# Performance work log

Hardware: AMD Instinct MI355X
Metric: run time of the kernel (lower is better)

Reference implementation:

```python
import jax, jax.numpy as jnp
import numpy as np

ED = 1024
NH = 16
HD = ED // NH


def setup_inputs() -> dict:
    key = jax.random.key(0)
    ks = jax.random.split(key, 9)
    s = 1.0 / np.sqrt(ED)
    return {
        "x": jax.random.normal(ks[0], (2, 2048, ED), dtype=jnp.float32),
        "wq": jax.random.uniform(ks[1], (ED, ED), jnp.float32, -s, s),
        "bq": jax.random.uniform(ks[2], (ED,), jnp.float32, -s, s),
        "wk": jax.random.uniform(ks[3], (ED, ED), jnp.float32, -s, s),
        "bk": jax.random.uniform(ks[4], (ED,), jnp.float32, -s, s),
        "wv": jax.random.uniform(ks[5], (ED, ED), jnp.float32, -s, s),
        "bv": jax.random.uniform(ks[6], (ED,), jnp.float32, -s, s),
        "wo": jax.random.uniform(ks[7], (ED, ED), jnp.float32, -s, s),
        "bo": jax.random.uniform(ks[8], (ED,), jnp.float32, -s, s),
    }


def reference(x, wq, bq, wk, bk, wv, bv, wo, bo):
    B, N, _ = x.shape
    # projections; weights stored as [out, in] like nn.Linear -> x @ W.T + b
    def proj(w, b):
        y = jnp.einsum('bnd,ed->bne', x, w) + b
        return y.reshape(B, N, NH, HD).transpose(0, 2, 1, 3)  # [B, H, N, hd]
    Q, K, V = proj(wq, bq), proj(wk, bk), proj(wv, bv)
    scores = jnp.einsum('bhnd,bhmd->bhnm', Q, K) / jnp.sqrt(jnp.float32(HD))
    attn = jax.nn.softmax(scores, axis=-1)
    ctx = jnp.einsum('bhnm,bhmd->bhnd', attn, V)
    ctx = ctx.transpose(0, 2, 1, 3).reshape(B, N, ED)
    return jnp.einsum('bne,de->bnd', ctx, wo) + bo
```

## Files before the change

### kernel.cpp

```cpp
#include <hip/hip_runtime.h>
#include <hip/hip_bf16.h>

#define ED 1024
#define NH 16
#define HD 64
#define SEQ 2048

typedef float f32x4 __attribute__((ext_vector_type(4)));
typedef float f32x16 __attribute__((ext_vector_type(16)));
typedef short s16x8 __attribute__((ext_vector_type(8)));
typedef short s16x4 __attribute__((ext_vector_type(4)));
typedef __attribute__((address_space(1))) const unsigned int GBuf;
typedef __attribute__((address_space(3))) unsigned int LBuf;

#define QSC 0.18033688011112042f

union BF8 { s16x8 v; __hip_bfloat16 h[8]; };

__device__ __forceinline__ unsigned cvt_pk_bf16(float lo, float hi) {
  unsigned r;
  asm("v_cvt_pk_bf16_f32 %0, %1, %2" : "=v"(r) : "v"(lo), "v"(hi));
  return r;
}

__device__ __forceinline__ s16x8 pack_pfrag(float p0, float p1, float p2, float p3,
                                            float p4, float p5, float p6, float p7) {
  unsigned w0 = cvt_pk_bf16(p0, p1), w1 = cvt_pk_bf16(p2, p3);
  unsigned w2 = cvt_pk_bf16(p4, p5), w3 = cvt_pk_bf16(p6, p7);
  asm("v_permlane32_swap_b32 %0, %1" : "+v"(w0), "+v"(w2));
  asm("v_permlane32_swap_b32 %0, %1" : "+v"(w1), "+v"(w3));
  union { unsigned u[4]; s16x8 v; } r;
  r.u[0] = w0; r.u[1] = w1; r.u[2] = w2; r.u[3] = w3;
  return r.v;
}

__device__ inline void cvt_one(const float* __restrict__ s, __hip_bfloat16* __restrict__ d,
                               int n, int t, int stride) {
  const int n8 = n >> 3;
  for (int i = t; i < n8; i += stride) {
    const float4 u = ((const float4*)s)[2 * i];
    const float4 v = ((const float4*)s)[2 * i + 1];
    BF8 o;
    o.h[0] = __float2bfloat16(u.x); o.h[1] = __float2bfloat16(u.y);
    o.h[2] = __float2bfloat16(u.z); o.h[3] = __float2bfloat16(u.w);
    o.h[4] = __float2bfloat16(v.x); o.h[5] = __float2bfloat16(v.y);
    o.h[6] = __float2bfloat16(v.z); o.h[7] = __float2bfloat16(v.w);
    ((s16x8*)d)[i] = o.v;
  }
}

__global__ __launch_bounds__(256) void cvt5(const float* s0, const float* s1, const float* s2,
                                            const float* s3, const float* s4,
                                            __hip_bfloat16* d0, __hip_bfloat16* d1,
                                            __hip_bfloat16* d2, __hip_bfloat16* d3,
                                            __hip_bfloat16* d4,
                                            int n0, int n1, int n2, int n3, int n4) {
  const int stride = gridDim.x * blockDim.x;
  const int t = blockIdx.x * blockDim.x + threadIdx.x;
  cvt_one(s0, d0, n0, t, stride);
  cvt_one(s1, d1, n1, t, stride);
  cvt_one(s2, d2, n2, t, stride);
  cvt_one(s3, d3, n3, t, stride);
  cvt_one(s4, d4, n4, t, stride);
}

__global__ __launch_bounds__(256) void gemm_qkv(const __hip_bfloat16* __restrict__ A,
                                                const __hip_bfloat16* __restrict__ wq,
                                                const float* __restrict__ bq,
                                                const __hip_bfloat16* __restrict__ wk,
                                                const float* __restrict__ bk,
                                                const __hip_bfloat16* __restrict__ wv,
                                                const float* __restrict__ bv,
                                                __hip_bfloat16* __restrict__ Qo,
                                                __hip_bfloat16* __restrict__ Ko,
                                                __hip_bfloat16* __restrict__ Vo) {
  __shared__ __hip_bfloat16 As[128 * 64];
  __shared__ __hip_bfloat16 Bs[128 * 64];

  const int z = blockIdx.z;
  const __hip_bfloat16* W = (z == 0) ? wq : (z == 1) ? wk : wv;
  const float* bias = (z == 0) ? bq : (z == 1) ? bk : bv;

  const int tid = threadIdx.x;
  const int wave = tid >> 6, lane = tid & 63;
  const int ln15 = lane & 15, lg = lane >> 4;
  const int m0 = blockIdx.y * 128, n0 = blockIdx.x * 128;
  const int wr = (wave >> 1) * 64, wc = (wave & 1) * 64;

  f32x4 acc[4][4];
#pragma unroll
  for (int i = 0; i < 4; i++)
#pragma unroll
    for (int j = 0; j < 4; j++) acc[i][j] = (f32x4){0.f, 0.f, 0.f, 0.f};

  const int srow = tid >> 3;
  const int sk = (tid & 7) * 8;

  for (int k0 = 0; k0 < ED; k0 += 64) {
    __syncthreads();
#pragma unroll
    for (int c = 0; c < 4; c++) {
      const int r = c * 32 + srow;
      __builtin_amdgcn_global_load_lds((GBuf*)(A + (size_t)(m0 + r) * ED + k0 + sk),
                                       (LBuf*)((char*)As + c * 4096 + tid * 16), 16, 0, 0);
    }
#pragma unroll
    for (int c = 0; c < 4; c++) {
      const int r = c * 32 + srow;
      __builtin_amdgcn_global_load_lds((GBuf*)(W + (size_t)(n0 + r) * ED + k0 + sk),
                                       (LBuf*)((char*)Bs + c * 4096 + tid * 16), 16, 0, 0);
    }
    __syncthreads();
#pragma unroll
    for (int kb = 0; kb < 2; kb++) {
      const int kof = kb * 32 + lg * 8;
      s16x8 a[4], b[4];
#pragma unroll
      for (int i = 0; i < 4; i++)
        a[i] = *(const s16x8*)&As[(wr + i * 16 + ln15) * 64 + kof];
#pragma unroll
      for (int j = 0; j < 4; j++)
        b[j] = *(const s16x8*)&Bs[(wc + j * 16 + ln15) * 64 + kof];
#pragma unroll
      for (int i = 0; i < 4; i++)
#pragma unroll
        for (int j = 0; j < 4; j++)
          acc[i][j] = __builtin_amdgcn_mfma_f32_16x16x32_bf16(a[i], b[j], acc[i][j], 0, 0, 0);
    }
  }

  const float scale = (z == 0) ? QSC : 1.0f;
  if (z < 2) {
    __hip_bfloat16* out = (z == 0) ? Qo : Ko;
#pragma unroll
    for (int j = 0; j < 4; j++) {
      const int e = n0 + wc + j * 16 + ln15;
      const float bvv = bias[e];
      const int h = e >> 6, hd = e & 63;
#pragma unroll
      for (int i = 0; i < 4; i++) {
#pragma unroll
        for (int r = 0; r < 4; r++) {
          const int m = m0 + wr + i * 16 + lg * 4 + r;
          const int b = m >> 11, n = m & 2047;
          out[(((size_t)(b * NH + h)) * SEQ + n) * HD + hd] =
              __float2bfloat16((acc[i][j][r] + bvv) * scale);
        }
      }
    }
  } else {
#pragma unroll
    for (int j = 0; j < 4; j++) {
      const int e = n0 + wc + j * 16 + ln15;
      const float bvv = bias[e];
      const int h = e >> 6, hd = e & 63;
#pragma unroll
      for (int i = 0; i < 4; i++) {
        const int m = m0 + wr + i * 16 + lg * 4;
        const int b = m >> 11, n = m & 2047;
        union { s16x4 v; __hip_bfloat16 hh[4]; } pk;
#pragma unroll
        for (int r = 0; r < 4; r++) pk.hh[r] = __float2bfloat16(acc[i][j][r] + bvv);
        *(s16x4*)&Vo[(((size_t)(b * NH + h)) * HD + hd) * SEQ + n] = pk.v;
      }
    }
  }
}

__global__ __launch_bounds__(256) void gemm_out(const __hip_bfloat16* __restrict__ A,
                                                const __hip_bfloat16* __restrict__ W,
                                                const float* __restrict__ bias,
                                                float* __restrict__ out) {
  __shared__ __hip_bfloat16 As[128 * 64];
  __shared__ __hip_bfloat16 Bs[128 * 64];

  const int tid = threadIdx.x;
  const int wave = tid >> 6, lane = tid & 63;
  const int ln15 = lane & 15, lg = lane >> 4;
  const int m0 = blockIdx.y * 128, n0 = blockIdx.x * 128;
  const int wr = (wave >> 1) * 64, wc = (wave & 1) * 64;

  f32x4 acc[4][4];
#pragma unroll
  for (int i = 0; i < 4; i++)
#pragma unroll
    for (int j = 0; j < 4; j++) acc[i][j] = (f32x4){0.f, 0.f, 0.f, 0.f};

  const int srow = tid >> 3;
  const int sk = (tid & 7) * 8;

  for (int k0 = 0; k0 < ED; k0 += 64) {
    __syncthreads();
#pragma unroll
    for (int c = 0; c < 4; c++) {
      const int r = c * 32 + srow;
      __builtin_amdgcn_global_load_lds((GBuf*)(A + (size_t)(m0 + r) * ED + k0 + sk),
                                       (LBuf*)((char*)As + c * 4096 + tid * 16), 16, 0, 0);
    }
#pragma unroll
    for (int c = 0; c < 4; c++) {
      const int r = c * 32 + srow;
      __builtin_amdgcn_global_load_lds((GBuf*)(W + (size_t)(n0 + r) * ED + k0 + sk),
                                       (LBuf*)((char*)Bs + c * 4096 + tid * 16), 16, 0, 0);
    }
    __syncthreads();
#pragma unroll
    for (int kb = 0; kb < 2; kb++) {
      const int kof = kb * 32 + lg * 8;
      s16x8 a[4], b[4];
#pragma unroll
      for (int i = 0; i < 4; i++)
        a[i] = *(const s16x8*)&As[(wr + i * 16 + ln15) * 64 + kof];
#pragma unroll
      for (int j = 0; j < 4; j++)
        b[j] = *(const s16x8*)&Bs[(wc + j * 16 + ln15) * 64 + kof];
#pragma unroll
      for (int i = 0; i < 4; i++)
#pragma unroll
        for (int j = 0; j < 4; j++)
          acc[i][j] = __builtin_amdgcn_mfma_f32_16x16x32_bf16(a[i], b[j], acc[i][j], 0, 0, 0);
    }
  }

#pragma unroll
  for (int j = 0; j < 4; j++) {
    const int e = n0 + wc + j * 16 + ln15;
    const float bvv = bias[e];
#pragma unroll
    for (int i = 0; i < 4; i++)
#pragma unroll
      for (int r = 0; r < 4; r++) {
        const int m = m0 + wr + i * 16 + lg * 4 + r;
        out[(size_t)m * ED + e] = acc[i][j][r] + bvv;
      }
  }
}

__global__ __launch_bounds__(256) void attn_bf16(const __hip_bfloat16* __restrict__ Q,
                                                 const __hip_bfloat16* __restrict__ K,
                                                 const __hip_bfloat16* __restrict__ VT,
                                                 __hip_bfloat16* __restrict__ CTX) {
  __shared__ __hip_bfloat16 KsS[2][64 * 64];
  __shared__ __hip_bfloat16 VtS[2][64 * 64];

  const int tid = threadIdx.x;
  const int wave = tid >> 6, lane = tid & 63;
  const int l31 = lane & 31, hi = lane >> 5;
  const int rswz = l31 & 7;

  const int bid = blockIdx.x;
  const int work = (bid & 7) * 64 + (bid >> 3);
  const int qb = work & 15;
  const int bh = work >> 4;

  const __hip_bfloat16* Qh = Q + (size_t)bh * SEQ * HD;
  const __hip_bfloat16* Kh = K + (size_t)bh * SEQ * HD;
  const __hip_bfloat16* Vh = VT + (size_t)bh * HD * SEQ;

  const int q0 = qb * 128 + wave * 32;

  s16x8 aq[4];
#pragma unroll
  for (int kb = 0; kb < 4; kb++)
    aq[kb] = *(const s16x8*)&Qh[(size_t)(q0 + l31) * HD + kb * 16 + hi * 8];

  f32x16 acc0 = {}, acc1 = {};
  float m_ = -1e30f, l_ = 0.f;

  auto STAGE = [&](int kt_, int buf_) {
#pragma unroll
    for (int c = 0; c < 2; c++) {
      const int row = c * 32 + (tid >> 3);
      const int colb = ((tid & 7) * 16) ^ ((row & 7) << 4);
      __builtin_amdgcn_global_load_lds(
          (GBuf*)((const char*)Kh + ((size_t)(kt_ * 64 + row) * HD) * 2 + colb),
          (LBuf*)((char*)&KsS[buf_][0] + c * 4096 + tid * 16), 16, 0, 0);
      __builtin_amdgcn_global_load_lds(
          (GBuf*)((const char*)Vh + ((size_t)row * SEQ + kt_ * 64) * 2 + colb),
          (LBuf*)((char*)&VtS[buf_][0] + c * 4096 + tid * 16), 16, 0, 0);
    }
  };

  STAGE(0, 0);

  const int NT = SEQ / 64;
  for (int kt = 0; kt < NT; kt++) {
    const int cur = kt & 1;
    __syncthreads();
    if (kt + 1 < NT) STAGE(kt + 1, cur ^ 1);

    f32x16 s0 = {}, s1 = {};
#pragma unroll
    for (int kb = 0; kb < 4; kb++) {
      const int coff = ((kb * 2 + hi) ^ rswz) << 4;
      const s16x8 ak0 = *(const s16x8*)((const char*)&KsS[cur][0] + l31 * 128 + coff);
      const s16x8 ak1 = *(const s16x8*)((const char*)&KsS[cur][0] + (32 + l31) * 128 + coff);
      s0 = __builtin_amdgcn_mfma_f32_32x32x16_bf16(ak0, aq[kb], s0, 0, 0, 0);
      s1 = __builtin_amdgcn_mfma_f32_32x32x16_bf16(ak1, aq[kb], s1, 0, 0, 0);
    }

    float t8[8];
#pragma unroll
    for (int i = 0; i < 8; i++)
      t8[i] = fmaxf(fmaxf(s0[i], s0[i + 8]), fmaxf(s1[i], s1[i + 8]));
    float tm = fmaxf(fmaxf(fmaxf(t8[0], t8[1]), fmaxf(t8[2], t8[3])),
                     fmaxf(fmaxf(t8[4], t8[5]), fmaxf(t8[6], t8[7])));
    tm = fmaxf(tm, __shfl_xor(tm, 32));

    if (!__all(tm - m_ <= 8.0f)) {
      const float mnew = fmaxf(m_, tm);
      const float fs = exp2f(m_ - mnew);
      m_ = mnew;
      l_ *= fs;
#pragma unroll
      for (int r = 0; r < 16; r++) { acc0[r] *= fs; acc1[r] *= fs; }
    }

#pragma unroll
    for (int r = 0; r < 16; r++) {
      s0[r] = exp2f(s0[r] - m_);
      s1[r] = exp2f(s1[r] - m_);
    }
    float sa[8];
#pragma unroll
    for (int i = 0; i < 8; i++) sa[i] = (s0[i] + s0[i + 8]) + (s1[i] + s1[i + 8]);
    float sum = ((sa[0] + sa[1]) + (sa[2] + sa[3])) + ((sa[4] + sa[5]) + (sa[6] + sa[7]));
    sum += __shfl_xor(sum, 32);
    l_ += sum;

    s16x8 pa[4];
    pa[0] = pack_pfrag(s0[0], s0[1], s0[2], s0[3], s0[4], s0[5], s0[6], s0[7]);
    pa[1] = pack_pfrag(s0[8], s0[9], s0[10], s0[11], s0[12], s0[13], s0[14], s0[15]);
    pa[2] = pack_pfrag(s1[0], s1[1], s1[2], s1[3], s1[4], s1[5], s1[6], s1[7]);
    pa[3] = pack_pfrag(s1[8], s1[9], s1[10], s1[11], s1[12], s1[13], s1[14], s1[15]);

#pragma unroll
    for (int kp = 0; kp < 4; kp++) {
      const int coff = ((kp * 2 + hi) ^ rswz) << 4;
      const s16x8 av0 = *(const s16x8*)((const char*)&VtS[cur][0] + l31 * 128 + coff);
      const s16x8 av1 = *(const s16x8*)((const char*)&VtS[cur][0] + (32 + l31) * 128 + coff);
      acc0 = __builtin_amdgcn_mfma_f32_32x32x16_bf16(av0, pa[kp], acc0, 0, 0, 0);
      acc1 = __builtin_amdgcn_mfma_f32_32x32x16_bf16(av1, pa[kp], acc1, 0, 0, 0);
    }
  }

  const float inv = 1.0f / l_;
  const int b = bh / NH, h = bh % NH;
  const int n = q0 + l31;
  __hip_bfloat16* dst = &CTX[((size_t)(b * SEQ + n)) * ED + h * HD];
#pragma unroll
  for (int g = 0; g < 4; g++) {
    union { s16x4 v; __hip_bfloat16 hh[4]; } p0, p1;
#pragma unroll
    for (int r = 0; r < 4; r++) {
      p0.hh[r] = __float2bfloat16(acc0[4 * g + r] * inv);
      p1.hh[r] = __float2bfloat16(acc1[4 * g + r] * inv);
    }
    *(s16x4*)&dst[8 * g + 4 * hi] = p0.v;
    *(s16x4*)&dst[32 + 8 * g + 4 * hi] = p1.v;
  }
}

extern "C" void kernel_launch(void* const* d_in, const int* in_sizes, int n_in,
                              void* d_out, int out_size, void* d_ws, size_t ws_size,
                              hipStream_t stream) {
  const float* x = (const float*)d_in[0];
  const float* wq = (const float*)d_in[1];
  const float* bq = (const float*)d_in[2];
  const float* wk = (const float*)d_in[3];
  const float* bk = (const float*)d_in[4];
  const float* wv = (const float*)d_in[5];
  const float* bv = (const float*)d_in[6];
  const float* wo = (const float*)d_in[7];
  const float* bo = (const float*)d_in[8];
  float* out = (float*)d_out;

  const int BN = in_sizes[0] / ED;

  char* w = (char*)d_ws;
  __hip_bfloat16* xbf = (__hip_bfloat16*)(w);
  __hip_bfloat16* wqb = (__hip_bfloat16*)(w + (8 << 20));
  __hip_bfloat16* wkb = (__hip_bfloat16*)(w + (10 << 20));
  __hip_bfloat16* wvb = (__hip_bfloat16*)(w + (12 << 20));
  __hip_bfloat16* wob = (__hip_bfloat16*)(w + (14 << 20));
  __hip_bfloat16* Qb = (__hip_bfloat16*)(w + (16 << 20));
  __hip_bfloat16* Kb = (__hip_bfloat16*)(w + (24 << 20));
  __hip_bfloat16* VTb = (__hip_bfloat16*)(w + (32 << 20));
  __hip_bfloat16* CTXb = (__hip_bfloat16*)(w + (40 << 20));

  cvt5<<<1024, 256, 0, stream>>>(x, wq, wk, wv, wo, xbf, wqb, wkb, wvb, wob,
                                 BN * ED, ED * ED, ED * ED, ED * ED, ED * ED);

  const dim3 blk(256);
  gemm_qkv<<<dim3(ED / 128, BN / 128, 3), blk, 0, stream>>>(
      xbf, wqb, bq, wkb, bk, wvb, bv, Qb, Kb, VTb);

  attn_bf16<<<dim3(512), blk, 0, stream>>>(Qb, Kb, VTb, CTXb);

  gemm_out<<<dim3(ED / 128, BN / 128), blk, 0, stream>>>(CTXb, wob, bo, out);
}
```

Measured before the change: 243.8 us.

## Double-buffer GEMM tiles, triple-buffer attention K/V, remap blocks, add wave priorities

Both projection GEMMs now double-buffer their A and B tiles in LDS, so the next k-tile loads while MFMAs run on the current one, with one barrier per iteration. Block indices are remapped so consecutive blocks share weight columns, aiming for better L2 reuse. The attention kernel moves to a three-stage K/V ring that prefetches two tiles ahead, using an explicit vmcnt wait and a raw barrier, and MFMA sections are wrapped in s_setprio. This doubles GEMM LDS use and raises attention LDS use, which can lower occupancy, and the hand-written vmcnt count must match the number of outstanding loads per stage.

```diff
diff --git a/kernel.cpp b/kernel.cpp
--- a/kernel.cpp
+++ b/kernel.cpp
@@ -74,17 +74,21 @@
                                                 __hip_bfloat16* __restrict__ Qo,
                                                 __hip_bfloat16* __restrict__ Ko,
                                                 __hip_bfloat16* __restrict__ Vo) {
-  __shared__ __hip_bfloat16 As[128 * 64];
-  __shared__ __hip_bfloat16 Bs[128 * 64];
-
-  const int z = blockIdx.z;
+  __shared__ __hip_bfloat16 As[2][128 * 64];
+  __shared__ __hip_bfloat16 Bs[2][128 * 64];
+
+  const int lin = (blockIdx.z * 32 + blockIdx.y) * 8 + blockIdx.x;
+  const int work = (lin & 7) * 96 + (lin >> 3);
+  const int z = work >> 8;
+  const int rem = work & 255;
+  const int m0 = (rem >> 3) * 128, n0 = (rem & 7) * 128;
+
   const __hip_bfloat16* W = (z == 0) ? wq : (z == 1) ? wk : wv;
   const float* bias = (z == 0) ? bq : (z == 1) ? bk : bv;
 
   const int tid = threadIdx.x;
   const int wave = tid >> 6, lane = tid & 63;
   const int ln15 = lane & 15, lg = lane >> 4;
-  const int m0 = blockIdx.y * 128, n0 = blockIdx.x * 128;
   const int wr = (wave >> 1) * 64, wc = (wave & 1) * 64;
 
   f32x4 acc[4][4];
@@ -96,37 +100,43 @@
   const int srow = tid >> 3;
   const int sk = (tid & 7) * 8;
 
-  for (int k0 = 0; k0 < ED; k0 += 64) {
-    __syncthreads();
+  auto STAGE = [&](int t, int buf) {
+    const int k0 = t * 64;
 #pragma unroll
     for (int c = 0; c < 4; c++) {
       const int r = c * 32 + srow;
       __builtin_amdgcn_global_load_lds((GBuf*)(A + (size_t)(m0 + r) * ED + k0 + sk),
-                                       (LBuf*)((char*)As + c * 4096 + tid * 16), 16, 0, 0);
-    }
-#pragma unroll
-    for (int c = 0; c < 4; c++) {
-      const int r = c * 32 + srow;
+                                       (LBuf*)((char*)&As[buf][0] + c * 4096 + tid * 16), 16, 0, 0);
       __builtin_amdgcn_global_load_lds((GBuf*)(W + (size_t)(n0 + r) * ED + k0 + sk),
-                                       (LBuf*)((char*)Bs + c * 4096 + tid * 16), 16, 0, 0);
-    }
-    __syncthreads();
+                                       (LBuf*)((char*)&Bs[buf][0] + c * 4096 + tid * 16), 16, 0, 0);
+    }
+  };
+
+  const int NT = ED / 64;
+  STAGE(0, 0);
+  __syncthreads();
+  for (int t = 0; t < NT; t++) {
+    const int cur = t & 1;
+    if (t + 1 < NT) STAGE(t + 1, cur ^ 1);
+    __builtin_amdgcn_s_setprio(1);
 #pragma unroll
     for (int kb = 0; kb < 2; kb++) {
       const int kof = kb * 32 + lg * 8;
       s16x8 a[4], b[4];
 #pragma unroll
       for (int i = 0; i < 4; i++)
-        a[i] = *(const s16x8*)&As[(wr + i * 16 + ln15) * 64 + kof];
+        a[i] = *(const s16x8*)&As[cur][(wr + i * 16 + ln15) * 64 + kof];
 #pragma unroll
       for (int j = 0; j < 4; j++)
-        b[j] = *(const s16x8*)&Bs[(wc + j * 16 + ln15) * 64 + kof];
+        b[j] = *(const s16x8*)&Bs[cur][(wc + j * 16 + ln15) * 64 + kof];
 #pragma unroll
       for (int i = 0; i < 4; i++)
 #pragma unroll
         for (int j = 0; j < 4; j++)
           acc[i][j] = __builtin_amdgcn_mfma_f32_16x16x32_bf16(a[i], b[j], acc[i][j], 0, 0, 0);
     }
+    __builtin_amdgcn_s_setprio(0);
+    __syncthreads();
   }
 
   const float scale = (z == 0) ? QSC : 1.0f;
@@ -171,13 +181,16 @@
                                                 const __hip_bfloat16* __restrict__ W,
                                                 const float* __restrict__ bias,
                                                 float* __restrict__ out) {
-  __shared__ __hip_bfloat16 As[128 * 64];
-  __shared__ __hip_bfloat16 Bs[128 * 64];
+  __shared__ __hip_bfloat16 As[2][128 * 64];
+  __shared__ __hip_bfloat16 Bs[2][128 * 64];
+
+  const int lin = blockIdx.y * 8 + blockIdx.x;
+  const int work = (lin & 7) * 32 + (lin >> 3);
+  const int m0 = (work >> 3) * 128, n0 = (work & 7) * 128;
 
   const int tid = threadIdx.x;
   const int wave = tid >> 6, lane = tid & 63;
   const int ln15 = lane & 15, lg = lane >> 4;
-  const int m0 = blockIdx.y * 128, n0 = blockIdx.x * 128;
   const int wr = (wave >> 1) * 64, wc = (wave & 1) * 64;
 
   f32x4 acc[4][4];
@@ -189,37 +202,43 @@
   const int srow = tid >> 3;
   const int sk = (tid & 7) * 8;
 
-  for (int k0 = 0; k0 < ED; k0 += 64) {
-    __syncthreads();
+  auto STAGE = [&](int t, int buf) {
+    const int k0 = t * 64;
 #pragma unroll
     for (int c = 0; c < 4; c++) {
       const int r = c * 32 + srow;
       __builtin_amdgcn_global_load_lds((GBuf*)(A + (size_t)(m0 + r) * ED + k0 + sk),
-                                       (LBuf*)((char*)As + c * 4096 + tid * 16), 16, 0, 0);
-    }
-#pragma unroll
-    for (int c = 0; c < 4; c++) {
-      const int r = c * 32 + srow;
+                                       (LBuf*)((char*)&As[buf][0] + c * 4096 + tid * 16), 16, 0, 0);
       __builtin_amdgcn_global_load_lds((GBuf*)(W + (size_t)(n0 + r) * ED + k0 + sk),
-                                       (LBuf*)((char*)Bs + c * 4096 + tid * 16), 16, 0, 0);
-    }
-    __syncthreads();
+                                       (LBuf*)((char*)&Bs[buf][0] + c * 4096 + tid * 16), 16, 0, 0);
+    }
+  };
+
+  const int NT = ED / 64;
+  STAGE(0, 0);
+  __syncthreads();
+  for (int t = 0; t < NT; t++) {
+    const int cur = t & 1;
+    if (t + 1 < NT) STAGE(t + 1, cur ^ 1);
+    __builtin_amdgcn_s_setprio(1);
 #pragma unroll
     for (int kb = 0; kb < 2; kb++) {
       const int kof = kb * 32 + lg * 8;
       s16x8 a[4], b[4];
 #pragma unroll
       for (int i = 0; i < 4; i++)
-        a[i] = *(const s16x8*)&As[(wr + i * 16 + ln15) * 64 + kof];
+        a[i] = *(const s16x8*)&As[cur][(wr + i * 16 + ln15) * 64 + kof];
 #pragma unroll
       for (int j = 0; j < 4; j++)
-        b[j] = *(const s16x8*)&Bs[(wc + j * 16 + ln15) * 64 + kof];
+        b[j] = *(const s16x8*)&Bs[cur][(wc + j * 16 + ln15) * 64 + kof];
 #pragma unroll
       for (int i = 0; i < 4; i++)
 #pragma unroll
         for (int j = 0; j < 4; j++)
           acc[i][j] = __builtin_amdgcn_mfma_f32_16x16x32_bf16(a[i], b[j], acc[i][j], 0, 0, 0);
     }
+    __builtin_amdgcn_s_setprio(0);
+    __syncthreads();
   }
 
 #pragma unroll
@@ -240,8 +259,8 @@
                                                  const __hip_bfloat16* __restrict__ K,
                                                  const __hip_bfloat16* __restrict__ VT,
                                                  __hip_bfloat16* __restrict__ CTX) {
-  __shared__ __hip_bfloat16 KsS[2][64 * 64];
-  __shared__ __hip_bfloat16 VtS[2][64 * 64];
+  __shared__ __hip_bfloat16 KsS[3][64 * 64];
+  __shared__ __hip_bfloat16 VtS[3][64 * 64];
 
   const int tid = threadIdx.x;
   const int wave = tid >> 6, lane = tid & 63;
@@ -281,15 +300,23 @@
     }
   };
 
+  const int NT = SEQ / 64;
   STAGE(0, 0);
-
-  const int NT = SEQ / 64;
+  STAGE(1, 1);
+
   for (int kt = 0; kt < NT; kt++) {
-    const int cur = kt & 1;
-    __syncthreads();
-    if (kt + 1 < NT) STAGE(kt + 1, cur ^ 1);
+    const int cur = kt % 3;
+    if (kt < NT - 1) {
+      asm volatile("s_waitcnt vmcnt(4)" ::: "memory");
+    } else {
+      asm volatile("s_waitcnt vmcnt(0)" ::: "memory");
+    }
+    __builtin_amdgcn_sched_barrier(0);
+    __builtin_amdgcn_s_barrier();
+    if (kt + 2 < NT) STAGE(kt + 2, (kt + 2) % 3);
 
     f32x16 s0 = {}, s1 = {};
+    __builtin_amdgcn_s_setprio(1);
 #pragma unroll
     for (int kb = 0; kb < 4; kb++) {
       const int coff = ((kb * 2 + hi) ^ rswz) << 4;
@@ -298,6 +325,7 @@
       s0 = __builtin_amdgcn_mfma_f32_32x32x16_bf16(ak0, aq[kb], s0, 0, 0, 0);
       s1 = __builtin_amdgcn_mfma_f32_32x32x16_bf16(ak1, aq[kb], s1, 0, 0, 0);
     }
+    __builtin_amdgcn_s_setprio(0);
 
     float t8[8];
 #pragma unroll
@@ -334,6 +362,7 @@
     pa[2] = pack_pfrag(s1[0], s1[1], s1[2], s1[3], s1[4], s1[5], s1[6], s1[7]);
     pa[3] = pack_pfrag(s1[8], s1[9], s1[10], s1[11], s1[12], s1[13], s1[14], s1[15]);
 
+    __builtin_amdgcn_s_setprio(1);
 #pragma unroll
     for (int kp = 0; kp < 4; kp++) {
       const int coff = ((kp * 2 + hi) ^ rswz) << 4;
@@ -342,6 +371,7 @@
       acc0 = __builtin_amdgcn_mfma_f32_32x32x16_bf16(av0, pa[kp], acc0, 0, 0, 0);
       acc1 = __builtin_amdgcn_mfma_f32_32x32x16_bf16(av1, pa[kp], acc1, 0, 0, 0);
     }
+    __builtin_amdgcn_s_setprio(0);
   }
 
   const float inv = 1.0f / l_;
```

New measurement: 237.7 us. 1.03x faster.
